# Performance work log

Measured on AMD Instinct MI355X. Metric: run time of the kernel, lower is better.

## Reference

```python
import jax, jax.numpy as jnp
import numpy as np

N_NODES = 50000
N_EDGES = 800000
IN_DIM = 128
HEADS = 4
OUT_DIM = 16
HD = HEADS * OUT_DIM  # 64
EDGE_DIM = 1
NEG_SLOPE = 0.2


def setup_inputs() -> dict:
    key = jax.random.key(0)
    ks = jax.random.split(key, 12)
    x = jax.random.normal(ks[0], (N_NODES, IN_DIM), dtype=jnp.float32)
    edge_index = jax.random.randint(ks[1], (2, N_EDGES), 0, N_NODES, dtype=jnp.int64)
    edge_attr = jax.random.uniform(ks[2], (N_EDGES, EDGE_DIM), dtype=jnp.float32)
    s = 0.1
    Wl = jax.random.normal(ks[3], (IN_DIM, HD), dtype=jnp.float32) * s
    bl = jax.random.normal(ks[4], (HD,), dtype=jnp.float32) * s
    Wr = jax.random.normal(ks[5], (IN_DIM, HD), dtype=jnp.float32) * s
    br = jax.random.normal(ks[6], (HD,), dtype=jnp.float32) * s
    We = jax.random.normal(ks[7], (EDGE_DIM, HD), dtype=jnp.float32) * s
    att = jax.random.normal(ks[8], (HEADS, OUT_DIM), dtype=jnp.float32) * s
    bias_out = jax.random.normal(ks[9], (HD,), dtype=jnp.float32) * s
    Wres = jax.random.normal(ks[10], (IN_DIM, HD), dtype=jnp.float32) * s
    bres = jax.random.normal(ks[11], (HD,), dtype=jnp.float32) * s
    return {"x": x, "edge_index": edge_index, "edge_attr": edge_attr,
            "Wl": Wl, "bl": bl, "Wr": Wr, "br": br, "We": We,
            "att": att, "bias_out": bias_out, "Wres": Wres, "bres": bres}


def _gatv2_layer(x, edge_index, edge_attr, Wl, bl, Wr, br, We, att, bias_out, Wres, bres):
    src, dst = edge_index[0], edge_index[1]
    # projections: [N, H, D]
    x_l = (x @ Wl + bl).reshape(N_NODES, HEADS, OUT_DIM)
    x_r = (x @ Wr + br).reshape(N_NODES, HEADS, OUT_DIM)
    edge_emb = (edge_attr @ We).reshape(N_EDGES, HEADS, OUT_DIM)
    # per-edge attention score (GATv2): a^T LeakyReLU(x_l[src] + x_r[dst] + e)
    x_j = x_l[src]                                   # [E, H, D] gather (source message)
    feat = x_j + x_r[dst] + edge_emb                 # [E, H, D]
    score = jnp.einsum('ehd,hd->eh', jax.nn.leaky_relu(feat, NEG_SLOPE), att)  # [E, H]
    # segment softmax over destination neighborhoods
    m = jax.ops.segment_max(score, dst, num_segments=N_NODES)   # [N, H]
    ex = jnp.exp(score - m[dst])                                 # [E, H]
    denom = jax.ops.segment_sum(ex, dst, num_segments=N_NODES)  # [N, H]
    alpha = ex / (denom[dst] + 1e-16)                            # [E, H]
    # scatter-add aggregation of weighted source messages
    out = jax.ops.segment_sum(alpha[:, :, None] * x_j, dst, num_segments=N_NODES)  # [N, H, D]
    out = out.reshape(N_NODES, HD) + bias_out        # concat heads + conv bias
    # residual (in_dim != out_features -> linear projection), then ELU
    out = out + (x @ Wres + bres)
    out = jax.nn.elu(out)
    return out, edge_index, alpha


def reference(x, edge_index, edge_attr, Wl, bl, Wr, br, We, att, bias_out, Wres, bres):
    return _gatv2_layer(x, edge_index, edge_attr, Wl, bl, Wr, br, We, att, bias_out, Wres, bres)
```

## Files before the change

kernel.cpp:

```cpp
#include <hip/hip_runtime.h>
#include <math.h>

#define N_NODES 50000
#define N_EDGES 800000
#define IN_DIM  128
#define HEADS   4
#define OUT_DIM 16
#define HD      64
#define NEG_SLOPE 0.2f
#define CAP     128
#define LOG2E   1.44269504088896340736f

__device__ __forceinline__ float hw_exp2(float x) {
    return __builtin_amdgcn_exp2f(x);
}

__global__ __launch_bounds__(256)
void k1_proj(const float* __restrict__ x,
             const float* __restrict__ Wl, const float* __restrict__ bl,
             const float* __restrict__ Wr, const float* __restrict__ br,
             const float* __restrict__ Wres, const float* __restrict__ bres,
             int* __restrict__ count,
             float* __restrict__ xl, float* __restrict__ xr,
             float* __restrict__ xres) {
    __shared__ float xsT[IN_DIM][36];
    const int base = blockIdx.x * 32;

    const int gid = blockIdx.x * 256 + threadIdx.x;
    if (gid < N_NODES) count[gid] = 0;

    {
        const float4* x4 = (const float4*)x;
#pragma unroll
        for (int r = 0; r < 4; ++r) {
            const int E    = threadIdx.x * 4 + r;
            const int node = E >> 5;
            const int kq   = E & 31;
            float4 v = make_float4(0.f, 0.f, 0.f, 0.f);
            if (base + node < N_NODES) v = x4[(size_t)(base + node) * 32 + kq];
            xsT[4 * kq + 0][node] = v.x;
            xsT[4 * kq + 1][node] = v.y;
            xsT[4 * kq + 2][node] = v.z;
            xsT[4 * kq + 3][node] = v.w;
        }
    }
    __syncthreads();

    const int lane = threadIdx.x & 63;
    const int wv   = threadIdx.x >> 6;
    const int u    = lane & 15;
    const int g    = lane >> 4;
    const int n0   = wv * 8;

    float4 aL[8], aR[8], aS[8];
#pragma unroll
    for (int i = 0; i < 8; ++i) {
        aL[i] = make_float4(0.f, 0.f, 0.f, 0.f);
        aR[i] = make_float4(0.f, 0.f, 0.f, 0.f);
        aS[i] = make_float4(0.f, 0.f, 0.f, 0.f);
    }

    const float* pL = Wl   + g * HD + 4 * u;
    const float* pR = Wr   + g * HD + 4 * u;
    const float* pS = Wres + g * HD + 4 * u;

#pragma unroll 2
    for (int k0 = 0; k0 < IN_DIM; k0 += 4) {
        const int k = k0 + g;
        const float4 wl4 = *(const float4*)(pL + k0 * HD);
        const float4 wr4 = *(const float4*)(pR + k0 * HD);
        const float4 ws4 = *(const float4*)(pS + k0 * HD);
        const float4 xa  = *(const float4*)&xsT[k][n0];
        const float4 xb  = *(const float4*)&xsT[k][n0 + 4];
        const float xn[8] = {xa.x, xa.y, xa.z, xa.w, xb.x, xb.y, xb.z, xb.w};
#pragma unroll
        for (int i = 0; i < 8; ++i) {
            aL[i].x += xn[i] * wl4.x; aL[i].y += xn[i] * wl4.y;
            aL[i].z += xn[i] * wl4.z; aL[i].w += xn[i] * wl4.w;
            aR[i].x += xn[i] * wr4.x; aR[i].y += xn[i] * wr4.y;
            aR[i].z += xn[i] * wr4.z; aR[i].w += xn[i] * wr4.w;
            aS[i].x += xn[i] * ws4.x; aS[i].y += xn[i] * ws4.y;
            aS[i].z += xn[i] * ws4.z; aS[i].w += xn[i] * ws4.w;
        }
    }

#pragma unroll
    for (int off = 16; off <= 32; off <<= 1) {
#pragma unroll
        for (int i = 0; i < 8; ++i) {
            aL[i].x += __shfl_xor(aL[i].x, off); aL[i].y += __shfl_xor(aL[i].y, off);
            aL[i].z += __shfl_xor(aL[i].z, off); aL[i].w += __shfl_xor(aL[i].w, off);
            aR[i].x += __shfl_xor(aR[i].x, off); aR[i].y += __shfl_xor(aR[i].y, off);
            aR[i].z += __shfl_xor(aR[i].z, off); aR[i].w += __shfl_xor(aR[i].w, off);
            aS[i].x += __shfl_xor(aS[i].x, off); aS[i].y += __shfl_xor(aS[i].y, off);
            aS[i].z += __shfl_xor(aS[i].z, off); aS[i].w += __shfl_xor(aS[i].w, off);
        }
    }

    if (g == 0) {
        const float4 bl4 = *(const float4*)(bl   + 4 * u);
        const float4 br4 = *(const float4*)(br   + 4 * u);
        const float4 bs4 = *(const float4*)(bres + 4 * u);
#pragma unroll
        for (int i = 0; i < 8; ++i) {
            const int node = base + n0 + i;
            if (node < N_NODES) {
                float4 o;
                const size_t off0 = (size_t)node * HD + 4 * u;
                o.x = aL[i].x + bl4.x; o.y = aL[i].y + bl4.y;
                o.z = aL[i].z + bl4.z; o.w = aL[i].w + bl4.w;
                *(float4*)(xl + off0) = o;
                o.x = aR[i].x + br4.x; o.y = aR[i].y + br4.y;
                o.z = aR[i].z + br4.z; o.w = aR[i].w + br4.w;
                *(float4*)(xr + off0) = o;
                o.x = aS[i].x + bs4.x; o.y = aS[i].y + bs4.y;
                o.z = aS[i].z + bs4.z; o.w = aS[i].w + bs4.w;
                *(float4*)(xres + off0) = o;
            }
        }
    }
}

__global__ __launch_bounds__(256)
void k2_hist(const int* __restrict__ dst, int* __restrict__ count,
             int* __restrict__ rank) {
    int e = blockIdx.x * blockDim.x + threadIdx.x;
    if (e < N_EDGES) rank[e] = atomicAdd(&count[dst[e]], 1);
}

#define SCAN_BLOCKS 196

__global__ __launch_bounds__(256)
void k3a_scan1(const int* __restrict__ count, int* __restrict__ incl,
               int* __restrict__ bsum) {
    __shared__ int s[256];
    const int t = threadIdx.x;
    const int i = blockIdx.x * 256 + t;
    int c = (i < N_NODES) ? count[i] : 0;
    s[t] = c;
    __syncthreads();
    for (int off = 1; off < 256; off <<= 1) {
        int v = (t >= off) ? s[t - off] : 0;
        __syncthreads();
        s[t] += v;
        __syncthreads();
    }
    if (i < N_NODES) incl[i] = s[t];
    if (t == 255) bsum[blockIdx.x] = s[255];
}

__global__ __launch_bounds__(256)
void k3b_scan2(int* __restrict__ bsum, int* __restrict__ boff) {
    __shared__ int s[256];
    const int t = threadIdx.x;
    int c = (t < SCAN_BLOCKS) ? bsum[t] : 0;
    s[t] = c;
    __syncthreads();
    for (int off = 1; off < 256; off <<= 1) {
        int v = (t >= off) ? s[t - off] : 0;
        __syncthreads();
        s[t] += v;
        __syncthreads();
    }
    if (t < SCAN_BLOCKS) boff[t] = s[t] - c;
}

__global__ __launch_bounds__(256)
void k3c_scan3(const int* __restrict__ count, int* __restrict__ incl ,
               const int* __restrict__ boff) {
    const int i = blockIdx.x * 256 + threadIdx.x;
    if (i >= N_NODES) return;
    incl[i] = incl[i] - count[i] + boff[blockIdx.x];
}

__global__ __launch_bounds__(256)
void k4_scatter(const int* __restrict__ src, const int* __restrict__ dst,
                const float* __restrict__ ea, const int* __restrict__ rank,
                const int* __restrict__ rowptr, int4* __restrict__ recs,
                float* __restrict__ out_ei) {
    int e = blockIdx.x * blockDim.x + threadIdx.x;
    if (e >= N_EDGES) return;
    const int d = dst[e];
    const int s = src[e];
    const int pos = rowptr[d] + rank[e];
    recs[pos] = make_int4(e, s, __float_as_int(ea[e]), 0);
    out_ei[e] = (float)s;
    out_ei[N_EDGES + e] = (float)d;
}

__global__ __launch_bounds__(256)
void k5_node(const int4* __restrict__ recs,
             const int* __restrict__ rowptr, const int* __restrict__ count,
             const float* __restrict__ xl, const float* __restrict__ xr,
             const float* __restrict__ xres,
             const float* __restrict__ We, const float* __restrict__ att,
             const float* __restrict__ bias_out,
             float* __restrict__ out, float* __restrict__ out_alpha) {
    __shared__ float sc_lds[4][CAP][HEADS];

    const int wv   = threadIdx.x >> 6;
    const int lane = threadIdx.x & 63;
    const int u    = lane & 7;
    const int g    = lane >> 3;
    const int n    = blockIdx.x * 4 + wv;

    const int base = rowptr[n];
    const int deg  = count[n];

    const float4 xrA = *(const float4*)(xr + (size_t)n * HD + 8 * u);
    const float4 xrB = *(const float4*)(xr + (size_t)n * HD + 8 * u + 4);
    const float4 WeA = *(const float4*)(We + 8 * u);
    const float4 WeB = *(const float4*)(We + 8 * u + 4);
    float4 atA = *(const float4*)(att + 8 * u);
    float4 atB = *(const float4*)(att + 8 * u + 4);
    atA.x *= LOG2E; atA.y *= LOG2E; atA.z *= LOG2E; atA.w *= LOG2E;
    atB.x *= LOG2E; atB.y *= LOG2E; atB.z *= LOG2E; atB.w *= LOG2E;

    float m = -INFINITY, dsum = 0.f;
    float4 accA = make_float4(0.f, 0.f, 0.f, 0.f);
    float4 accB = make_float4(0.f, 0.f, 0.f, 0.f);

    for (int c0 = 0; c0 < deg; c0 += 64) {
        const int nrem = min(64, deg - c0);
        int s_my = 0; float a_my = 0.f;
        if (lane < nrem) {
            const int4 r = recs[base + c0 + lane];
            s_my = r.y;
            a_my = __int_as_float(r.z);
        }
        const int nchunk = (nrem + 7) >> 3;

        int   j   = g;
        bool  v   = j < nrem;
        int   s   = __shfl(s_my, j);
        float aev = __shfl(a_my, j);
        float4 xlA = make_float4(0.f, 0.f, 0.f, 0.f);
        float4 xlB = make_float4(0.f, 0.f, 0.f, 0.f);
        if (v) {
            xlA = *(const float4*)(xl + (size_t)s * HD + 8 * u);
            xlB = *(const float4*)(xl + (size_t)s * HD + 8 * u + 4);
        }

        for (int c = 0; c < nchunk; ++c) {
            const float4 curA = xlA, curB = xlB;
            const bool   curv = v;
            const float  ca   = aev;
            const int    cj   = 8 * c + g;
            j = 8 * (c + 1) + g;
            v = j < nrem;
            s   = __shfl(s_my, j & 63);
            aev = __shfl(a_my, j & 63);
            if (v) {
                xlA = *(const float4*)(xl + (size_t)s * HD + 8 * u);
                xlB = *(const float4*)(xl + (size_t)s * HD + 8 * u + 4);
            }

            if (curv) {
                float f0 = curA.x + xrA.x + ca * WeA.x;
                float f1 = curA.y + xrA.y + ca * WeA.y;
                float f2 = curA.z + xrA.z + ca * WeA.z;
                float f3 = curA.w + xrA.w + ca * WeA.w;
                float f4 = curB.x + xrB.x + ca * WeB.x;
                float f5 = curB.y + xrB.y + ca * WeB.y;
                float f6 = curB.z + xrB.z + ca * WeB.z;
                float f7 = curB.w + xrB.w + ca * WeB.w;
                f0 = f0 > 0.f ? f0 : NEG_SLOPE * f0;
                f1 = f1 > 0.f ? f1 : NEG_SLOPE * f1;
                f2 = f2 > 0.f ? f2 : NEG_SLOPE * f2;
                f3 = f3 > 0.f ? f3 : NEG_SLOPE * f3;
                f4 = f4 > 0.f ? f4 : NEG_SLOPE * f4;
                f5 = f5 > 0.f ? f5 : NEG_SLOPE * f5;
                f6 = f6 > 0.f ? f6 : NEG_SLOPE * f6;
                f7 = f7 > 0.f ? f7 : NEG_SLOPE * f7;
                float p = f0 * atA.x + f1 * atA.y + f2 * atA.z + f3 * atA.w
                        + f4 * atB.x + f5 * atB.y + f6 * atB.z + f7 * atB.w;
                p += __shfl_xor(p, 1);
                const int jj = c0 + cj;
                if (jj < CAP && (u & 1) == 0) sc_lds[wv][jj][u >> 1] = p;
                const float t    = hw_exp2(-fabsf(p - m));
                const bool  up   = (p >= m);
                const float scl  = up ? t : 1.f;
                const float pe   = up ? 1.f : t;
                m = fmaxf(m, p);
                dsum  = dsum * scl + pe;
                accA.x = accA.x * scl + pe * curA.x;
                accA.y = accA.y * scl + pe * curA.y;
                accA.z = accA.z * scl + pe * curA.z;
                accA.w = accA.w * scl + pe * curA.w;
                accB.x = accB.x * scl + pe * curB.x;
                accB.y = accB.y * scl + pe * curB.y;
                accB.z = accB.z * scl + pe * curB.z;
                accB.w = accB.w * scl + pe * curB.w;
            }
        }
    }

#pragma unroll
    for (int off = 8; off <= 32; off <<= 1) {
        const float mo = __shfl_xor(m, off);
        const float d2 = __shfl_xor(dsum, off);
        float4 aA, aB;
        aA.x = __shfl_xor(accA.x, off); aA.y = __shfl_xor(accA.y, off);
        aA.z = __shfl_xor(accA.z, off); aA.w = __shfl_xor(accA.w, off);
        aB.x = __shfl_xor(accB.x, off); aB.y = __shfl_xor(accB.y, off);
        aB.z = __shfl_xor(accB.z, off); aB.w = __shfl_xor(accB.w, off);
        const float mm = fmaxf(m, mo);
        const float s1 = (m  == -INFINITY) ? 0.f : hw_exp2(m - mm);
        const float s2 = (mo == -INFINITY) ? 0.f : hw_exp2(mo - mm);
        dsum  = dsum * s1 + d2 * s2;
        accA.x = accA.x * s1 + aA.x * s2; accA.y = accA.y * s1 + aA.y * s2;
        accA.z = accA.z * s1 + aA.z * s2; accA.w = accA.w * s1 + aA.w * s2;
        accB.x = accB.x * s1 + aB.x * s2; accB.y = accB.y * s1 + aB.y * s2;
        accB.z = accB.z * s1 + aB.z * s2; accB.w = accB.w * s1 + aB.w * s2;
        m = mm;
    }
    const float inv = 1.f / (dsum + 1e-16f);

    const float m0 = __shfl(m, 0),  m1 = __shfl(m, 2);
    const float m2 = __shfl(m, 4),  m3 = __shfl(m, 6);
    const float i0 = __shfl(inv, 0), i1 = __shfl(inv, 2);
    const float i2 = __shfl(inv, 4), i3 = __shfl(inv, 6);

    __syncthreads();

    for (int jj = lane; jj < deg; jj += 64) {
        const int4 r = recs[base + jj];
        const int  e = r.x;
        float s0, s1, s2, s3;
        if (jj < CAP) {
            const float4 sc4 = *(const float4*)&sc_lds[wv][jj][0];
            s0 = sc4.x; s1 = sc4.y; s2 = sc4.z; s3 = sc4.w;
        } else {
            const int   sN  = r.y;
            const float aev = __int_as_float(r.z);
            float sc[4];
            for (int h2 = 0; h2 < 4; ++h2) {
                float a2 = 0.f;
                for (int d2 = 0; d2 < 16; ++d2) {
                    const int hd2 = h2 * 16 + d2;
                    float f = xl[(size_t)sN * HD + hd2] + xr[(size_t)n * HD + hd2]
                              + aev * We[hd2];
                    f = f > 0.f ? f : NEG_SLOPE * f;
                    a2 += f * att[hd2];
                }
                sc[h2] = a2 * LOG2E;
            }
            s0 = sc[0]; s1 = sc[1]; s2 = sc[2]; s3 = sc[3];
        }
        float4 a4;
        a4.x = hw_exp2(s0 - m0) * i0;
        a4.y = hw_exp2(s1 - m1) * i1;
        a4.z = hw_exp2(s2 - m2) * i2;
        a4.w = hw_exp2(s3 - m3) * i3;
        *(float4*)(out_alpha + (size_t)e * HEADS) = a4;
    }

    if (g == 0) {
        const float4 xsA = *(const float4*)(xres + (size_t)n * HD + 8 * u);
        const float4 xsB = *(const float4*)(xres + (size_t)n * HD + 8 * u + 4);
        const float4 bA  = *(const float4*)(bias_out + 8 * u);
        const float4 bB  = *(const float4*)(bias_out + 8 * u + 4);
        float4 o;
        o.x = accA.x * inv + bA.x + xsA.x;
        o.y = accA.y * inv + bA.y + xsA.y;
        o.z = accA.z * inv + bA.z + xsA.z;
        o.w = accA.w * inv + bA.w + xsA.w;
        o.x = o.x > 0.f ? o.x : __expf(o.x) - 1.f;
        o.y = o.y > 0.f ? o.y : __expf(o.y) - 1.f;
        o.z = o.z > 0.f ? o.z : __expf(o.z) - 1.f;
        o.w = o.w > 0.f ? o.w : __expf(o.w) - 1.f;
        *(float4*)(out + (size_t)n * HD + 8 * u) = o;
        o.x = accB.x * inv + bB.x + xsB.x;
        o.y = accB.y * inv + bB.y + xsB.y;
        o.z = accB.z * inv + bB.z + xsB.z;
        o.w = accB.w * inv + bB.w + xsB.w;
        o.x = o.x > 0.f ? o.x : __expf(o.x) - 1.f;
        o.y = o.y > 0.f ? o.y : __expf(o.y) - 1.f;
        o.z = o.z > 0.f ? o.z : __expf(o.z) - 1.f;
        o.w = o.w > 0.f ? o.w : __expf(o.w) - 1.f;
        *(float4*)(out + (size_t)n * HD + 8 * u + 4) = o;
    }
}

extern "C" void kernel_launch(void* const* d_in, const int* in_sizes, int n_in,
                              void* d_out, int out_size, void* d_ws, size_t ws_size,
                              hipStream_t stream) {
    const float* x        = (const float*)d_in[0];
    const int*   ei       = (const int*)d_in[1];
    const float* ea       = (const float*)d_in[2];
    const float* Wl       = (const float*)d_in[3];
    const float* bl       = (const float*)d_in[4];
    const float* Wr       = (const float*)d_in[5];
    const float* br       = (const float*)d_in[6];
    const float* We       = (const float*)d_in[7];
    const float* att      = (const float*)d_in[8];
    const float* bias_out = (const float*)d_in[9];
    const float* Wres     = (const float*)d_in[10];
    const float* bres     = (const float*)d_in[11];

    const int* src = ei;
    const int* dst = ei + N_EDGES;

    float* out       = (float*)d_out;
    float* out_ei    = out + (size_t)N_NODES * HD;
    float* out_alpha = out_ei + 2 * (size_t)N_EDGES;

    float* ws   = (float*)d_ws;
    float* xl   = ws;
    float* xr   = xl + (size_t)N_NODES * HD;
    float* xres = xr + (size_t)N_NODES * HD;
    int* ibuf   = (int*)(xres + (size_t)N_NODES * HD);
    int* count  = ibuf;
    int* rowptr = count + N_NODES;
    int* bsum   = rowptr + N_NODES;
    int* boff   = bsum + SCAN_BLOCKS;
    int* rank   = boff + SCAN_BLOCKS;
    size_t recoff = (size_t)(rank + N_EDGES - (int*)d_ws);
    recoff = (recoff + 3) & ~(size_t)3;
    int4* recs  = (int4*)((int*)d_ws + recoff);

    k1_proj<<<(N_NODES + 31) / 32, 256, 0, stream>>>(x, Wl, bl, Wr, br, Wres, bres,
                                                     count, xl, xr, xres);
    k2_hist<<<N_EDGES / 256, 256, 0, stream>>>(dst, count, rank);
    k3a_scan1<<<SCAN_BLOCKS, 256, 0, stream>>>(count, rowptr, bsum);
    k3b_scan2<<<1, 256, 0, stream>>>(bsum, boff);
    k3c_scan3<<<SCAN_BLOCKS, 256, 0, stream>>>(count, rowptr, boff);
    k4_scatter<<<(N_EDGES + 255) / 256, 256, 0, stream>>>(src, dst, ea, rank,
                                                          rowptr, recs, out_ei);
    k5_node<<<N_NODES / 4, 256, 0, stream>>>(recs, rowptr, count,
                                             xl, xr, xres, We, att, bias_out,
                                             out, out_alpha);
}
```

Measured before the change: 268.6 us.

## Store source projections in fp16 and defer online-softmax rescaling in gather loop

The source projection xl is now written in half precision, which halves the bytes gathered per edge in the node aggregation kernel. The online softmax now rescales its accumulators only when a new score exceeds the running max by more than a threshold, rather than on every edge. The running max starts at a finite value, so the infinity guards in the merge step are removed. The loop is also double-buffered so two gather loads are in flight. The cost is fp16 rounding of xl in both scores and messages, plus overflow risk if scores run far above the start value.

```diff
diff --git a/kernel.cpp b/kernel.cpp
--- a/kernel.cpp
+++ b/kernel.cpp
@@ -1,4 +1,5 @@
 #include <hip/hip_runtime.h>
+#include <hip/hip_fp16.h>
 #include <math.h>
 
 #define N_NODES 50000
@@ -10,6 +11,7 @@
 #define NEG_SLOPE 0.2f
 #define CAP     128
 #define LOG2E   1.44269504088896340736f
+#define DEFER_THR 8.0f
 
 __device__ __forceinline__ float hw_exp2(float x) {
     return __builtin_amdgcn_exp2f(x);
@@ -21,7 +23,7 @@
              const float* __restrict__ Wr, const float* __restrict__ br,
              const float* __restrict__ Wres, const float* __restrict__ bres,
              int* __restrict__ count,
-             float* __restrict__ xl, float* __restrict__ xr,
+             __half* __restrict__ xlh, float* __restrict__ xr,
              float* __restrict__ xres) {
     __shared__ float xsT[IN_DIM][36];
     const int base = blockIdx.x * 32;
@@ -105,11 +107,16 @@
         for (int i = 0; i < 8; ++i) {
             const int node = base + n0 + i;
             if (node < N_NODES) {
+                const size_t off0 = (size_t)node * HD + 4 * u;
+                const __half2 h0 = __float22half2_rn(
+                    make_float2(aL[i].x + bl4.x, aL[i].y + bl4.y));
+                const __half2 h1 = __float22half2_rn(
+                    make_float2(aL[i].z + bl4.z, aL[i].w + bl4.w));
+                uint2 pk;
+                pk.x = *(const unsigned int*)&h0;
+                pk.y = *(const unsigned int*)&h1;
+                *(uint2*)(xlh + off0) = pk;
                 float4 o;
-                const size_t off0 = (size_t)node * HD + 4 * u;
-                o.x = aL[i].x + bl4.x; o.y = aL[i].y + bl4.y;
-                o.z = aL[i].z + bl4.z; o.w = aL[i].w + bl4.w;
-                *(float4*)(xl + off0) = o;
                 o.x = aR[i].x + br4.x; o.y = aR[i].y + br4.y;
                 o.z = aR[i].z + br4.z; o.w = aR[i].w + br4.w;
                 *(float4*)(xr + off0) = o;
@@ -191,7 +198,7 @@
 __global__ __launch_bounds__(256)
 void k5_node(const int4* __restrict__ recs,
              const int* __restrict__ rowptr, const int* __restrict__ count,
-             const float* __restrict__ xl, const float* __restrict__ xr,
+             const __half* __restrict__ xlh, const float* __restrict__ xr,
              const float* __restrict__ xres,
              const float* __restrict__ We, const float* __restrict__ att,
              const float* __restrict__ bias_out,
@@ -216,9 +223,51 @@
     atA.x *= LOG2E; atA.y *= LOG2E; atA.z *= LOG2E; atA.w *= LOG2E;
     atB.x *= LOG2E; atB.y *= LOG2E; atB.z *= LOG2E; atB.w *= LOG2E;
 
-    float m = -INFINITY, dsum = 0.f;
+    float m = -128.f, dsum = 0.f;
     float4 accA = make_float4(0.f, 0.f, 0.f, 0.f);
     float4 accB = make_float4(0.f, 0.f, 0.f, 0.f);
+
+    auto PROCESS = [&](const float4& raw, float ca, int jj) {
+        const __half2* hp = (const __half2*)&raw;
+        const float2 p0 = __half22float2(hp[0]);
+        const float2 p1 = __half22float2(hp[1]);
+        const float2 p2 = __half22float2(hp[2]);
+        const float2 p3 = __half22float2(hp[3]);
+        float f0 = p0.x + xrA.x + ca * WeA.x;
+        float f1 = p0.y + xrA.y + ca * WeA.y;
+        float f2 = p1.x + xrA.z + ca * WeA.z;
+        float f3 = p1.y + xrA.w + ca * WeA.w;
+        float f4 = p2.x + xrB.x + ca * WeB.x;
+        float f5 = p2.y + xrB.y + ca * WeB.y;
+        float f6 = p3.x + xrB.z + ca * WeB.z;
+        float f7 = p3.y + xrB.w + ca * WeB.w;
+        f0 = fmaxf(f0, NEG_SLOPE * f0);
+        f1 = fmaxf(f1, NEG_SLOPE * f1);
+        f2 = fmaxf(f2, NEG_SLOPE * f2);
+        f3 = fmaxf(f3, NEG_SLOPE * f3);
+        f4 = fmaxf(f4, NEG_SLOPE * f4);
+        f5 = fmaxf(f5, NEG_SLOPE * f5);
+        f6 = fmaxf(f6, NEG_SLOPE * f6);
+        f7 = fmaxf(f7, NEG_SLOPE * f7);
+        float p = f0 * atA.x + f1 * atA.y + f2 * atA.z + f3 * atA.w
+                + f4 * atB.x + f5 * atB.y + f6 * atB.z + f7 * atB.w;
+        p += __shfl_xor(p, 1);
+        if (jj < CAP && (u & 1) == 0) sc_lds[wv][jj][u >> 1] = p;
+        const float diff = p - m;
+        if (diff > DEFER_THR) {
+            const float scl = hw_exp2(-diff);
+            dsum *= scl;
+            accA.x *= scl; accA.y *= scl; accA.z *= scl; accA.w *= scl;
+            accB.x *= scl; accB.y *= scl; accB.z *= scl; accB.w *= scl;
+            m = p;
+        }
+        const float pe = hw_exp2(p - m);
+        dsum += pe;
+        accA.x += pe * p0.x; accA.y += pe * p0.y;
+        accA.z += pe * p1.x; accA.w += pe * p1.y;
+        accB.x += pe * p2.x; accB.y += pe * p2.y;
+        accB.z += pe * p3.x; accB.w += pe * p3.y;
+    };
 
     for (int c0 = 0; c0 < deg; c0 += 64) {
         const int nrem = min(64, deg - c0);
@@ -230,67 +279,43 @@
         }
         const int nchunk = (nrem + 7) >> 3;
 
-        int   j   = g;
-        bool  v   = j < nrem;
-        int   s   = __shfl(s_my, j);
-        float aev = __shfl(a_my, j);
-        float4 xlA = make_float4(0.f, 0.f, 0.f, 0.f);
-        float4 xlB = make_float4(0.f, 0.f, 0.f, 0.f);
-        if (v) {
-            xlA = *(const float4*)(xl + (size_t)s * HD + 8 * u);
-            xlB = *(const float4*)(xl + (size_t)s * HD + 8 * u + 4);
-        }
-
-        for (int c = 0; c < nchunk; ++c) {
-            const float4 curA = xlA, curB = xlB;
-            const bool   curv = v;
-            const float  ca   = aev;
-            const int    cj   = 8 * c + g;
-            j = 8 * (c + 1) + g;
-            v = j < nrem;
-            s   = __shfl(s_my, j & 63);
-            aev = __shfl(a_my, j & 63);
-            if (v) {
-                xlA = *(const float4*)(xl + (size_t)s * HD + 8 * u);
-                xlB = *(const float4*)(xl + (size_t)s * HD + 8 * u + 4);
+        int   jA = g;
+        bool  vA = jA < nrem;
+        int   sA = __shfl(s_my, jA & 63);
+        float aA = __shfl(a_my, jA & 63);
+        float4 bufA = make_float4(0.f, 0.f, 0.f, 0.f);
+        if (vA) bufA = *(const float4*)(xlh + (size_t)sA * HD + 8 * u);
+        int   jB = 8 + g;
+        bool  vB = jB < nrem;
+        int   sB = __shfl(s_my, jB & 63);
+        float aB = __shfl(a_my, jB & 63);
+        float4 bufB = make_float4(0.f, 0.f, 0.f, 0.f);
+        if (vB) bufB = *(const float4*)(xlh + (size_t)sB * HD + 8 * u);
+
+        for (int c = 0; c < nchunk; c += 2) {
+            {
+                const float4 cur  = bufA;
+                const bool   curv = vA;
+                const float  ca   = aA;
+                const int    jj   = c0 + 8 * c + g;
+                jA = 8 * (c + 2) + g;
+                vA = jA < nrem;
+                sA = __shfl(s_my, jA & 63);
+                aA = __shfl(a_my, jA & 63);
+                if (vA) bufA = *(const float4*)(xlh + (size_t)sA * HD + 8 * u);
+                if (curv) PROCESS(cur, ca, jj);
             }
-
-            if (curv) {
-                float f0 = curA.x + xrA.x + ca * WeA.x;
-                float f1 = curA.y + xrA.y + ca * WeA.y;
-                float f2 = curA.z + xrA.z + ca * WeA.z;
-                float f3 = curA.w + xrA.w + ca * WeA.w;
-                float f4 = curB.x + xrB.x + ca * WeB.x;
-                float f5 = curB.y + xrB.y + ca * WeB.y;
-                float f6 = curB.z + xrB.z + ca * WeB.z;
-                float f7 = curB.w + xrB.w + ca * WeB.w;
-                f0 = f0 > 0.f ? f0 : NEG_SLOPE * f0;
-                f1 = f1 > 0.f ? f1 : NEG_SLOPE * f1;
-                f2 = f2 > 0.f ? f2 : NEG_SLOPE * f2;
-                f3 = f3 > 0.f ? f3 : NEG_SLOPE * f3;
-                f4 = f4 > 0.f ? f4 : NEG_SLOPE * f4;
-                f5 = f5 > 0.f ? f5 : NEG_SLOPE * f5;
-                f6 = f6 > 0.f ? f6 : NEG_SLOPE * f6;
-                f7 = f7 > 0.f ? f7 : NEG_SLOPE * f7;
-                float p = f0 * atA.x + f1 * atA.y + f2 * atA.z + f3 * atA.w
-                        + f4 * atB.x + f5 * atB.y + f6 * atB.z + f7 * atB.w;
-                p += __shfl_xor(p, 1);
-                const int jj = c0 + cj;
-                if (jj < CAP && (u & 1) == 0) sc_lds[wv][jj][u >> 1] = p;
-                const float t    = hw_exp2(-fabsf(p - m));
-                const bool  up   = (p >= m);
-                const float scl  = up ? t : 1.f;
-                const float pe   = up ? 1.f : t;
-                m = fmaxf(m, p);
-                dsum  = dsum * scl + pe;
-                accA.x = accA.x * scl + pe * curA.x;
-                accA.y = accA.y * scl + pe * curA.y;
-                accA.z = accA.z * scl + pe * curA.z;
-                accA.w = accA.w * scl + pe * curA.w;
-                accB.x = accB.x * scl + pe * curB.x;
-                accB.y = accB.y * scl + pe * curB.y;
-                accB.z = accB.z * scl + pe * curB.z;
-                accB.w = accB.w * scl + pe * curB.w;
+            {
+                const float4 cur  = bufB;
+                const bool   curv = vB;
+                const float  ca   = aB;
+                const int    jj   = c0 + 8 * (c + 1) + g;
+                jB = 8 * (c + 3) + g;
+                vB = jB < nrem;
+                sB = __shfl(s_my, jB & 63);
+                aB = __shfl(a_my, jB & 63);
+                if (vB) bufB = *(const float4*)(xlh + (size_t)sB * HD + 8 * u);
+                if (curv) PROCESS(cur, ca, jj);
             }
         }
     }
@@ -299,19 +324,19 @@
     for (int off = 8; off <= 32; off <<= 1) {
         const float mo = __shfl_xor(m, off);
         const float d2 = __shfl_xor(dsum, off);
-        float4 aA, aB;
-        aA.x = __shfl_xor(accA.x, off); aA.y = __shfl_xor(accA.y, off);
-        aA.z = __shfl_xor(accA.z, off); aA.w = __shfl_xor(accA.w, off);
-        aB.x = __shfl_xor(accB.x, off); aB.y = __shfl_xor(accB.y, off);
-        aB.z = __shfl_xor(accB.z, off); aB.w = __shfl_xor(accB.w, off);
+        float4 aA2, aB2;
+        aA2.x = __shfl_xor(accA.x, off); aA2.y = __shfl_xor(accA.y, off);
+        aA2.z = __shfl_xor(accA.z, off); aA2.w = __shfl_xor(accA.w, off);
+        aB2.x = __shfl_xor(accB.x, off); aB2.y = __shfl_xor(accB.y, off);
+        aB2.z = __shfl_xor(accB.z, off); aB2.w = __shfl_xor(accB.w, off);
         const float mm = fmaxf(m, mo);
-        const float s1 = (m  == -INFINITY) ? 0.f : hw_exp2(m - mm);
-        const float s2 = (mo == -INFINITY) ? 0.f : hw_exp2(mo - mm);
+        const float s1 = hw_exp2(m - mm);
+        const float s2 = hw_exp2(mo - mm);
         dsum  = dsum * s1 + d2 * s2;
-        accA.x = accA.x * s1 + aA.x * s2; accA.y = accA.y * s1 + aA.y * s2;
-        accA.z = accA.z * s1 + aA.z * s2; accA.w = accA.w * s1 + aA.w * s2;
-        accB.x = accB.x * s1 + aB.x * s2; accB.y = accB.y * s1 + aB.y * s2;
-        accB.z = accB.z * s1 + aB.z * s2; accB.w = accB.w * s1 + aB.w * s2;
+        accA.x = accA.x * s1 + aA2.x * s2; accA.y = accA.y * s1 + aA2.y * s2;
+        accA.z = accA.z * s1 + aA2.z * s2; accA.w = accA.w * s1 + aA2.w * s2;
+        accB.x = accB.x * s1 + aB2.x * s2; accB.y = accB.y * s1 + aB2.y * s2;
+        accB.z = accB.z * s1 + aB2.z * s2; accB.w = accB.w * s1 + aB2.w * s2;
         m = mm;
     }
     const float inv = 1.f / (dsum + 1e-16f);
@@ -338,9 +363,9 @@
                 float a2 = 0.f;
                 for (int d2 = 0; d2 < 16; ++d2) {
                     const int hd2 = h2 * 16 + d2;
-                    float f = xl[(size_t)sN * HD + hd2] + xr[(size_t)n * HD + hd2]
-                              + aev * We[hd2];
-                    f = f > 0.f ? f : NEG_SLOPE * f;
+                    float f = __half2float(xlh[(size_t)sN * HD + hd2])
+                              + xr[(size_t)n * HD + hd2] + aev * We[hd2];
+                    f = fmaxf(f, NEG_SLOPE * f);
                     a2 += f * att[hd2];
                 }
                 sc[h2] = a2 * LOG2E;
@@ -405,22 +430,22 @@
     float* out_ei    = out + (size_t)N_NODES * HD;
     float* out_alpha = out_ei + 2 * (size_t)N_EDGES;
 
-    float* ws   = (float*)d_ws;
-    float* xl   = ws;
-    float* xr   = xl + (size_t)N_NODES * HD;
-    float* xres = xr + (size_t)N_NODES * HD;
-    int* ibuf   = (int*)(xres + (size_t)N_NODES * HD);
-    int* count  = ibuf;
-    int* rowptr = count + N_NODES;
-    int* bsum   = rowptr + N_NODES;
-    int* boff   = bsum + SCAN_BLOCKS;
-    int* rank   = boff + SCAN_BLOCKS;
+    float* ws    = (float*)d_ws;
+    __half* xlh  = (__half*)ws;
+    float* xr    = ws + (size_t)N_NODES * HD / 2;
+    float* xres  = xr + (size_t)N_NODES * HD;
+    int* ibuf    = (int*)(xres + (size_t)N_NODES * HD);
+    int* count   = ibuf;
+    int* rowptr  = count + N_NODES;
+    int* bsum    = rowptr + N_NODES;
+    int* boff    = bsum + SCAN_BLOCKS;
+    int* rank    = boff + SCAN_BLOCKS;
     size_t recoff = (size_t)(rank + N_EDGES - (int*)d_ws);
     recoff = (recoff + 3) & ~(size_t)3;
     int4* recs  = (int4*)((int*)d_ws + recoff);
 
     k1_proj<<<(N_NODES + 31) / 32, 256, 0, stream>>>(x, Wl, bl, Wr, br, Wres, bres,
-                                                     count, xl, xr, xres);
+                                                     count, xlh, xr, xres);
     k2_hist<<<N_EDGES / 256, 256, 0, stream>>>(dst, count, rank);
     k3a_scan1<<<SCAN_BLOCKS, 256, 0, stream>>>(count, rowptr, bsum);
     k3b_scan2<<<1, 256, 0, stream>>>(bsum, boff);
@@ -428,6 +453,6 @@
     k4_scatter<<<(N_EDGES + 255) / 256, 256, 0, stream>>>(src, dst, ea, rank,
                                                           rowptr, recs, out_ei);
     k5_node<<<N_NODES / 4, 256, 0, stream>>>(recs, rowptr, count,
-                                             xl, xr, xres, We, att, bias_out,
+                                             xlh, xr, xres, We, att, bias_out,
                                              out, out_alpha);
 }
```

Result: faster. 262.8 us (-2.2%).
